# Performance work log

Hardware: AMD Instinct MI355X
Metric: run time of the kernel (lower is better)

## Reference

```python
import jax, jax.numpy as jnp
import numpy as np

DIM = 128
KS = 7
HEADS = 4
HEAD_DIM = DIM // HEADS


def setup_inputs() -> dict:
    key = jax.random.key(0)
    ks = jax.random.split(key, 10)
    B, H, W, C = 4, 64, 64, DIM
    s = 0.02
    return {
        "x": jax.random.normal(ks[0], (B, H, W, C), jnp.float32),
        "qkv_w": jax.random.normal(ks[1], (C, 3 * C), jnp.float32) * s,
        "qkv_b": jnp.zeros((3 * C,), jnp.float32),
        "proj_w": jax.random.normal(ks[2], (C, C), jnp.float32) * s,
        "proj_b": jnp.zeros((C,), jnp.float32),
        "rpb": jax.random.normal(ks[3], (HEADS, 2 * KS - 1, 2 * KS - 1), jnp.float32) * s,
        "g1_w": jax.random.normal(ks[4], (C, C // 2), jnp.float32) * s,
        "g1_b": jnp.zeros((C // 2,), jnp.float32),
        "g2_w": jax.random.normal(ks[5], (C // 2, 1), jnp.float32) * s,
        "g2_b": jnp.zeros((1,), jnp.float32),
    }


def _neighborhood_attention(x, qkv_w, qkv_b, proj_w, proj_b, rpb):
    B, H, W, C = x.shape
    k = KS
    # qkv projection -> [B,H,W,3,heads,head_dim]
    qkv = (x @ qkv_w + qkv_b).reshape(B, H, W, 3, HEADS, HEAD_DIM)
    q = qkv[..., 0, :, :] * (HEAD_DIM ** -0.5)  # [B,H,W,h,d]
    kk = qkv[..., 1, :, :]
    v = qkv[..., 2, :, :]

    # Clamped sliding-window start indices (NATTEN semantics)
    sh = jnp.clip(jnp.arange(H) - k // 2, 0, H - k)  # [H]
    sw = jnp.clip(jnp.arange(W) - k // 2, 0, W - k)  # [W]
    idx_h = sh[:, None] + jnp.arange(k)[None, :]  # [H,k]
    idx_w = sw[:, None] + jnp.arange(k)[None, :]  # [W,k]

    # Gather neighborhood windows: [B,H,W,k,k,h,d]
    kwin = kk[:, idx_h[:, None, :, None], idx_w[None, :, None, :]]
    vwin = v[:, idx_h[:, None, :, None], idx_w[None, :, None, :]]

    # Relative position bias indices: (neighbor - query) + (k-1)
    bih = idx_h - jnp.arange(H)[:, None] + (k - 1)  # [H,k]
    biw = idx_w - jnp.arange(W)[:, None] + (k - 1)  # [W,k]
    # bias: [h,H,W,k,k] -> [H,W,h,k,k]
    bias = rpb[:, bih[:, None, :, None], biw[None, :, None, :]]
    bias = jnp.transpose(bias, (1, 2, 0, 3, 4))

    # scores: [B,H,W,h,k,k]
    scores = jnp.einsum('bxyhd,bxyklhd->bxyhkl', q, kwin) + bias[None]
    attn = jax.nn.softmax(scores.reshape(B, H, W, HEADS, k * k), axis=-1)
    attn = attn.reshape(B, H, W, HEADS, k, k)
    out = jnp.einsum('bxyhkl,bxyklhd->bxyhd', attn, vwin).reshape(B, H, W, C)
    return out @ proj_w + proj_b


def reference(x, qkv_w, qkv_b, proj_w, proj_b, rpb, g1_w, g1_b, g2_w, g2_b):
    attn_out = _neighborhood_attention(x, qkv_w, qkv_b, proj_w, proj_b, rpb)
    gate = jax.nn.sigmoid(jax.nn.relu(x @ g1_w + g1_b) @ g2_w + g2_b)  # [B,H,W,1]
    return attn_out * gate + x
```

## Files before the change

### kernel.cpp

```cpp
#include <hip/hip_runtime.h>
#include <hip/hip_bf16.h>
#include <math.h>

#define PIXELS 16384
#define C      128
#define KS     7
#define HEADS  4
#define HD     32
#define QSCALE 0.17677669529663687f

typedef __bf16 bf16x8 __attribute__((ext_vector_type(8)));
typedef float  f32x4  __attribute__((ext_vector_type(4)));

__device__ inline unsigned short f2bf(float f) {
    unsigned int u = __builtin_bit_cast(unsigned int, f);
    u += 0x7FFFu + ((u >> 16) & 1u);
    return (unsigned short)(u >> 16);
}
__device__ inline float bflo(unsigned int u) {
    return __builtin_bit_cast(float, u << 16);
}
__device__ inline float bfhi(unsigned int u) {
    return __builtin_bit_cast(float, u & 0xFFFF0000u);
}

__global__ __launch_bounds__(256) void prep_kernel(
    const float* __restrict__ x, const float* __restrict__ qkv_w,
    const float* __restrict__ g1_w, const float* __restrict__ qkv_b,
    const float* __restrict__ g1_b, const float* __restrict__ proj_w,
    unsigned short* __restrict__ xb, unsigned short* __restrict__ wT,
    unsigned short* __restrict__ pT, float* __restrict__ bias_ext)
{
    const int blk = blockIdx.x, tid = threadIdx.x;
    if (blk < 2048) {
        int base = blk * 1024 + tid * 4;
        float4 v = *(const float4*)(x + base);
        ushort4 o; o.x = f2bf(v.x); o.y = f2bf(v.y); o.z = f2bf(v.z); o.w = f2bf(v.w);
        *(ushort4*)(xb + base) = o;
    } else if (blk < 2104) {
        int n = (blk - 2048) * 8 + (tid >> 5);
        int kq = tid & 31;
        float f0, f1, f2, f3;
        if (n < 384) {
            f0 = qkv_w[(kq*4+0)*384 + n]; f1 = qkv_w[(kq*4+1)*384 + n];
            f2 = qkv_w[(kq*4+2)*384 + n]; f3 = qkv_w[(kq*4+3)*384 + n];
        } else {
            int nn = n - 384;
            f0 = g1_w[(kq*4+0)*64 + nn]; f1 = g1_w[(kq*4+1)*64 + nn];
            f2 = g1_w[(kq*4+2)*64 + nn]; f3 = g1_w[(kq*4+3)*64 + nn];
        }
        ushort4 o; o.x = f2bf(f0); o.y = f2bf(f1); o.z = f2bf(f2); o.w = f2bf(f3);
        *(ushort4*)(wT + n*128 + kq*4) = o;
    } else if (blk < 2120) {
        int n = (blk - 2104) * 8 + (tid >> 5);
        int kq = tid & 31;
        ushort4 o;
        o.x = f2bf(proj_w[(kq*4+0)*128 + n]);
        o.y = f2bf(proj_w[(kq*4+1)*128 + n]);
        o.z = f2bf(proj_w[(kq*4+2)*128 + n]);
        o.w = f2bf(proj_w[(kq*4+3)*128 + n]);
        *(ushort4*)(pT + n*128 + kq*4) = o;
    } else {
        for (int idx = tid; idx < 448; idx += 256)
            bias_ext[idx] = (idx < 384) ? qkv_b[idx] : g1_b[idx - 384];
    }
}

__global__ __launch_bounds__(256) void gemm_qkvh_fused(
    const unsigned short* __restrict__ xb, const unsigned short* __restrict__ wT,
    const float* __restrict__ bias_ext, const float* __restrict__ g2_w,
    const float* __restrict__ g2_b, unsigned short* __restrict__ qkvb,
    float* __restrict__ gate)
{
    __shared__ __align__(16) unsigned short As[64*128];
    __shared__ __align__(16) unsigned short Bs[64*128];
    const int nt = blockIdx.x;
    const int n0 = nt * 64;
    const int m0 = blockIdx.y * 64;
    const int tid = threadIdx.x;

#pragma unroll
    for (int it = 0; it < 4; it++) {
        int idx = tid + it*256, row = idx >> 4, c = idx & 15;
        uint4 v = *(const uint4*)(xb + (size_t)(m0+row)*128 + c*8);
        *(uint4*)(As + row*128 + ((c ^ (row&7)) << 3)) = v;
    }
#pragma unroll
    for (int it = 0; it < 4; it++) {
        int idx = tid + it*256, row = idx >> 4, c = idx & 15;
        uint4 v = *(const uint4*)(wT + (size_t)(n0+row)*128 + c*8);
        *(uint4*)(Bs + row*128 + ((c ^ (row&7)) << 3)) = v;
    }
    __syncthreads();

    const int wave = tid >> 6, lane = tid & 63;
    const int l15 = lane & 15, quad = lane >> 4;
    const int wm = (wave & 1) * 32, wn = (wave >> 1) * 32;

    f32x4 acc[2][2] = {};
#pragma unroll
    for (int ks = 0; ks < 4; ks++) {
        bf16x8 af[2], bq[2];
#pragma unroll
        for (int mt = 0; mt < 2; mt++) {
            int m = wm + mt*16 + l15;
            af[mt] = *(const bf16x8*)(As + m*128 + (((ks*4+quad) ^ (m&7)) << 3));
        }
#pragma unroll
        for (int ntl = 0; ntl < 2; ntl++) {
            int n = wn + ntl*16 + l15;
            bq[ntl] = *(const bf16x8*)(Bs + n*128 + (((ks*4+quad) ^ (n&7)) << 3));
        }
#pragma unroll
        for (int mt = 0; mt < 2; mt++)
#pragma unroll
            for (int ntl = 0; ntl < 2; ntl++)
                acc[mt][ntl] = __builtin_amdgcn_mfma_f32_16x16x32_bf16(
                    af[mt], bq[ntl], acc[mt][ntl], 0, 0, 0);
    }
    __syncthreads();

    if (nt < 6) {
        unsigned short* Cs = (unsigned short*)As;
#pragma unroll
        for (int ntl = 0; ntl < 2; ntl++) {
            int nl = wn + ntl*16 + l15;
            int ng = n0 + nl;
            float qs = (ng < 128) ? QSCALE : 1.0f;
            float bv = bias_ext[ng];
#pragma unroll
            for (int mt = 0; mt < 2; mt++)
#pragma unroll
                for (int r = 0; r < 4; r++) {
                    int ml = wm + mt*16 + quad*4 + r;
                    Cs[ml*64 + nl] = f2bf((acc[mt][ntl][r] + bv) * qs);
                }
        }
        __syncthreads();
        int row = tid >> 2, part = tid & 3;
        uint4 a = *(const uint4*)(Cs + row*64 + part*16);
        uint4 b = *(const uint4*)(Cs + row*64 + part*16 + 8);
        unsigned short* dst = qkvb + (size_t)(m0+row)*384 + n0 + part*16;
        *(uint4*)dst = a;
        *(uint4*)(dst + 8) = b;
    } else {
        float* gpart = (float*)Bs;
        float rs[2][4];
#pragma unroll
        for (int mt = 0; mt < 2; mt++)
#pragma unroll
            for (int r = 0; r < 4; r++) rs[mt][r] = 0.0f;
#pragma unroll
        for (int ntl = 0; ntl < 2; ntl++) {
            int nl = wn + ntl*16 + l15;
            float bv = bias_ext[384 + nl];
            float gw = g2_w[nl];
#pragma unroll
            for (int mt = 0; mt < 2; mt++)
#pragma unroll
                for (int r = 0; r < 4; r++) {
                    float h = acc[mt][ntl][r] + bv;
                    rs[mt][r] += fmaxf(h, 0.0f) * gw;
                }
        }
#pragma unroll
        for (int off = 1; off <= 8; off <<= 1)
#pragma unroll
            for (int mt = 0; mt < 2; mt++)
#pragma unroll
                for (int r = 0; r < 4; r++)
                    rs[mt][r] += __shfl_xor(rs[mt][r], off);
        if (l15 == 0) {
#pragma unroll
            for (int mt = 0; mt < 2; mt++)
#pragma unroll
                for (int r = 0; r < 4; r++)
                    gpart[(wave >> 1)*64 + wm + mt*16 + quad*4 + r] = rs[mt][r];
        }
        __syncthreads();
        if (tid < 64) {
            float g = gpart[tid] + gpart[64 + tid] + g2_b[0];
            gate[m0 + tid] = 1.0f / (1.0f + __expf(-g));
        }
    }
}

__global__ __launch_bounds__(128) void attn_kernel(
    const unsigned short* __restrict__ qkvb, const float* __restrict__ rpb,
    unsigned short* __restrict__ attnb)
{
    __shared__ __align__(16) unsigned short kvs[196 * 136];
    __shared__ float rpb_lds[2 * 169];

    const int blk = blockIdx.x;
    const int pr = blk & 1;
    const int tile = (blk >> 1) & 63;
    const int b = blk >> 7;
    const int ti0 = (tile >> 3) * 8, tj0 = (tile & 7) * 8;
    int wr0 = ti0 - 3; if (wr0 < 0) wr0 = 0;
    int wc0 = tj0 - 3; if (wc0 < 0) wc0 = 0;

    const int tid = threadIdx.x;

    for (int t = tid; t < 338; t += 128) rpb_lds[t] = rpb[pr * 338 + t];

    for (int idx = tid; idx < 196 * 16; idx += 128) {
        int pos = idx >> 4, t = idx & 15;
        int wr = pos / 14, wc = pos - wr * 14;
        int gr = wr0 + wr; if (gr > 63) gr = 63;
        int gc = wc0 + wc; if (gc > 63) gc = 63;
        size_t gp = (size_t)(((b << 6) + gr) << 6) + gc;
        int src = 128 + ((t >> 3) << 7) + pr * 64 + ((t & 7) << 3);
        uint4 v = *(const uint4*)(qkvb + gp * 384 + src);
        *(uint4*)(kvs + pos * 136 + ((t >> 3) << 6) + ((t & 7) << 3)) = v;
    }
    __syncthreads();

    const int hh = tid >> 6, lane = tid & 63;
    const int h = pr * 2 + hh;
    const int pi = lane >> 3, pj = lane & 7;
    const int i = ti0 + pi, j = tj0 + pj;
    int sh = i - 3; sh = sh < 0 ? 0 : (sh > 57 ? 57 : sh);
    int sw = j - 3; sw = sw < 0 ? 0 : (sw > 57 ? 57 : sw);
    const int dr = sh - wr0, dc = sw - wc0;
    const size_t gp = (size_t)(((b << 6) + i) << 6) + j;

    unsigned int qu[16];
    const unsigned short* qptr = qkvb + gp * 384 + h * 32;
    *(uint4*)(qu + 0)  = *(const uint4*)(qptr + 0);
    *(uint4*)(qu + 4)  = *(const uint4*)(qptr + 8);
    *(uint4*)(qu + 8)  = *(const uint4*)(qptr + 16);
    *(uint4*)(qu + 12) = *(const uint4*)(qptr + 24);
    float qf[32];
#pragma unroll
    for (int p = 0; p < 16; p++) {
        qf[2*p]   = bflo(qu[p]);
        qf[2*p+1] = bfhi(qu[p]);
    }

    float acc[32];
#pragma unroll
    for (int d = 0; d < 32; d++) acc[d] = 0.0f;
    float ssum = 0.0f;

    const float* rl = rpb_lds + hh * 169;
    const int rbase = (sh - i + 6) * 13 + (sw - j + 6);
    const int hwbase = (dr * 14 + dc) * 136 + hh * 32;

    for (int kr = 0; kr < 7; kr++) {
        int hw = hwbase + kr * (14 * 136);
        int ri = rbase + kr * 13;
#pragma unroll
        for (int kc = 0; kc < 7; kc++) {
            const unsigned short* kp = kvs + hw;
            unsigned int ku[16];
            *(uint4*)(ku + 0)  = *(const uint4*)(kp + 0);
            *(uint4*)(ku + 4)  = *(const uint4*)(kp + 8);
            *(uint4*)(ku + 8)  = *(const uint4*)(kp + 16);
            *(uint4*)(ku + 12) = *(const uint4*)(kp + 24);
            float s0 = rl[ri + kc], s1 = 0.0f;
#pragma unroll
            for (int p = 0; p < 8; p++) {
                s0 += qf[2*p]      * bflo(ku[p])     + qf[2*p+1]  * bfhi(ku[p]);
                s1 += qf[2*p+16]   * bflo(ku[p+8])   + qf[2*p+17] * bfhi(ku[p+8]);
            }
            float e = __expf(s0 + s1);
            ssum += e;
            unsigned int vu[16];
            *(uint4*)(vu + 0)  = *(const uint4*)(kp + 64);
            *(uint4*)(vu + 4)  = *(const uint4*)(kp + 72);
            *(uint4*)(vu + 8)  = *(const uint4*)(kp + 80);
            *(uint4*)(vu + 12) = *(const uint4*)(kp + 88);
#pragma unroll
            for (int p = 0; p < 16; p++) {
                acc[2*p]   += e * bflo(vu[p]);
                acc[2*p+1] += e * bfhi(vu[p]);
            }
            hw += 136;
        }
    }

    const float inv = 1.0f / ssum;
    unsigned int o[16];
#pragma unroll
    for (int p = 0; p < 16; p++) {
        unsigned int lo = f2bf(acc[2*p] * inv);
        unsigned int hi = f2bf(acc[2*p+1] * inv);
        o[p] = lo | (hi << 16);
    }
    unsigned short* op = attnb + gp * 128 + h * 32;
    *(uint4*)(op + 0)  = *(const uint4*)(o + 0);
    *(uint4*)(op + 8)  = *(const uint4*)(o + 4);
    *(uint4*)(op + 16) = *(const uint4*)(o + 8);
    *(uint4*)(op + 24) = *(const uint4*)(o + 12);
}

__global__ __launch_bounds__(256) void gemm_proj_mfma(
    const unsigned short* __restrict__ ab, const unsigned short* __restrict__ pT,
    const float* __restrict__ proj_b, const float* __restrict__ gate,
    const float* __restrict__ x, float* __restrict__ out)
{
    __shared__ __align__(16) unsigned short As[64*128];
    __shared__ __align__(16) unsigned short Bs[64*128];
    const int n0 = blockIdx.x * 64;
    const int m0 = blockIdx.y * 64;
    const int tid = threadIdx.x;

#pragma unroll
    for (int it = 0; it < 4; it++) {
        int idx = tid + it*256, row = idx >> 4, c = idx & 15;
        uint4 v = *(const uint4*)(ab + (size_t)(m0+row)*128 + c*8);
        *(uint4*)(As + row*128 + ((c ^ (row&7)) << 3)) = v;
    }
#pragma unroll
    for (int it = 0; it < 4; it++) {
        int idx = tid + it*256, row = idx >> 4, c = idx & 15;
        uint4 v = *(const uint4*)(pT + (size_t)(n0+row)*128 + c*8);
        *(uint4*)(Bs + row*128 + ((c ^ (row&7)) << 3)) = v;
    }
    __syncthreads();

    const int wave = tid >> 6, lane = tid & 63;
    const int l15 = lane & 15, quad = lane >> 4;
    const int wm = (wave & 1) * 32, wn = (wave >> 1) * 32;

    f32x4 acc[2][2] = {};
#pragma unroll
    for (int ks = 0; ks < 4; ks++) {
        bf16x8 af[2], bq[2];
#pragma unroll
        for (int mt = 0; mt < 2; mt++) {
            int m = wm + mt*16 + l15;
            af[mt] = *(const bf16x8*)(As + m*128 + (((ks*4+quad) ^ (m&7)) << 3));
        }
#pragma unroll
        for (int ntl = 0; ntl < 2; ntl++) {
            int n = wn + ntl*16 + l15;
            bq[ntl] = *(const bf16x8*)(Bs + n*128 + (((ks*4+quad) ^ (n&7)) << 3));
        }
#pragma unroll
        for (int mt = 0; mt < 2; mt++)
#pragma unroll
            for (int ntl = 0; ntl < 2; ntl++)
                acc[mt][ntl] = __builtin_amdgcn_mfma_f32_16x16x32_bf16(
                    af[mt], bq[ntl], acc[mt][ntl], 0, 0, 0);
    }
    __syncthreads();

    float* Cs = (float*)As;
#pragma unroll
    for (int ntl = 0; ntl < 2; ntl++) {
        int nl = wn + ntl*16 + l15;
        float bv = proj_b[n0 + nl];
#pragma unroll
        for (int mt = 0; mt < 2; mt++)
#pragma unroll
            for (int r = 0; r < 4; r++) {
                int ml = wm + mt*16 + quad*4 + r;
                Cs[ml*64 + nl] = acc[mt][ntl][r] + bv;
            }
    }
    __syncthreads();
    int row = tid >> 2, part = tid & 3;
    float gv = gate[m0 + row];
    const float* xr = x + (size_t)(m0+row)*128 + n0 + part*16;
    float* orow = out + (size_t)(m0+row)*128 + n0 + part*16;
#pragma unroll
    for (int q = 0; q < 4; q++) {
        float4 cv = *(const float4*)(Cs + row*64 + part*16 + q*4);
        float4 xv = *(const float4*)(xr + q*4);
        float4 o;
        o.x = cv.x * gv + xv.x; o.y = cv.y * gv + xv.y;
        o.z = cv.z * gv + xv.z; o.w = cv.w * gv + xv.w;
        *(float4*)(orow + q*4) = o;
    }
}

extern "C" void kernel_launch(void* const* d_in, const int* in_sizes, int n_in,
                              void* d_out, int out_size, void* d_ws, size_t ws_size,
                              hipStream_t stream)
{
    const float* x      = (const float*)d_in[0];
    const float* qkv_w  = (const float*)d_in[1];
    const float* qkv_b  = (const float*)d_in[2];
    const float* proj_w = (const float*)d_in[3];
    const float* proj_b = (const float*)d_in[4];
    const float* rpb    = (const float*)d_in[5];
    const float* g1_w   = (const float*)d_in[6];
    const float* g1_b   = (const float*)d_in[7];
    const float* g2_w   = (const float*)d_in[8];
    const float* g2_b   = (const float*)d_in[9];
    float* out = (float*)d_out;

    float* ws        = (float*)d_ws;
    float* gate      = ws;
    float* bias_ext  = gate + 16384;
    unsigned short* xb    = (unsigned short*)(bias_ext + 448);
    unsigned short* wT    = xb + 2097152;
    unsigned short* pT    = wT + 57344;
    unsigned short* qkvb  = pT + 16384;
    unsigned short* attnb = qkvb + 6291456;

    (void)in_sizes; (void)n_in; (void)out_size; (void)ws_size;

    prep_kernel<<<2121, 256, 0, stream>>>(x, qkv_w, g1_w, qkv_b, g1_b, proj_w,
                                          xb, wT, pT, bias_ext);
    gemm_qkvh_fused<<<dim3(7, 256), 256, 0, stream>>>(xb, wT, bias_ext,
                                                      g2_w, g2_b, qkvb, gate);
    attn_kernel<<<512, 128, 0, stream>>>(qkvb, rpb, attnb);
    gemm_proj_mfma<<<dim3(2, 256), 256, 0, stream>>>(attnb, pT, proj_b, gate, x, out);
}
```

Measured before the change: 125.1 us.

## Split attention per head per block and divide window rows across two waves

Each attention block now handles a single head instead of a head pair, so twice as many blocks launch and each stages half as much K/V into LDS. The two waves in a block split the seven kernel rows between them, and partial sums are combined through LDS. The QK dot product uses the bf16 fdot2 builtin when it is available. The aim is more parallelism and occupancy plus cheaper score math, at the cost of an extra LDS reduction, a second barrier, and one idle wave during the final write.

```diff
diff --git a/kernel.cpp b/kernel.cpp
--- a/kernel.cpp
+++ b/kernel.cpp
@@ -10,6 +10,7 @@
 #define QSCALE 0.17677669529663687f
 
 typedef __bf16 bf16x8 __attribute__((ext_vector_type(8)));
+typedef __bf16 bf16x2 __attribute__((ext_vector_type(2)));
 typedef float  f32x4  __attribute__((ext_vector_type(4)));
 
 __device__ inline unsigned short f2bf(float f) {
@@ -189,35 +190,34 @@
     const unsigned short* __restrict__ qkvb, const float* __restrict__ rpb,
     unsigned short* __restrict__ attnb)
 {
-    __shared__ __align__(16) unsigned short kvs[196 * 136];
-    __shared__ float rpb_lds[2 * 169];
+    __shared__ __align__(16) unsigned short kvs[196 * 68];
+    __shared__ float rpb_lds[169];
 
     const int blk = blockIdx.x;
-    const int pr = blk & 1;
-    const int tile = (blk >> 1) & 63;
-    const int b = blk >> 7;
-    const int ti0 = (tile >> 3) * 8, tj0 = (tile & 7) * 8;
+    const int h = blk & 3;
+    const int tile = (blk >> 2) & 63;
+    const int b = blk >> 8;
+    const int ti0 = ((tile >> 3) << 3), tj0 = ((tile & 7) << 3);
     int wr0 = ti0 - 3; if (wr0 < 0) wr0 = 0;
     int wc0 = tj0 - 3; if (wc0 < 0) wc0 = 0;
 
     const int tid = threadIdx.x;
 
-    for (int t = tid; t < 338; t += 128) rpb_lds[t] = rpb[pr * 338 + t];
-
-    for (int idx = tid; idx < 196 * 16; idx += 128) {
-        int pos = idx >> 4, t = idx & 15;
+    for (int t = tid; t < 169; t += 128) rpb_lds[t] = rpb[h * 169 + t];
+
+    for (int idx = tid; idx < 196 * 8; idx += 128) {
+        int pos = idx >> 3, t = idx & 7;
         int wr = pos / 14, wc = pos - wr * 14;
         int gr = wr0 + wr; if (gr > 63) gr = 63;
         int gc = wc0 + wc; if (gc > 63) gc = 63;
         size_t gp = (size_t)(((b << 6) + gr) << 6) + gc;
-        int src = 128 + ((t >> 3) << 7) + pr * 64 + ((t & 7) << 3);
+        int src = 128 + ((t >> 2) << 7) + h * 32 + ((t & 3) << 3);
         uint4 v = *(const uint4*)(qkvb + gp * 384 + src);
-        *(uint4*)(kvs + pos * 136 + ((t >> 3) << 6) + ((t & 7) << 3)) = v;
-    }
-    __syncthreads();
-
-    const int hh = tid >> 6, lane = tid & 63;
-    const int h = pr * 2 + hh;
+        *(uint4*)(kvs + pos * 68 + ((t >> 2) << 5) + ((t & 3) << 3)) = v;
+    }
+    __syncthreads();
+
+    const int ww = tid >> 6, lane = tid & 63;
     const int pi = lane >> 3, pj = lane & 7;
     const int i = ti0 + pi, j = tj0 + pj;
     int sh = i - 3; sh = sh < 0 ? 0 : (sh > 57 ? 57 : sh);
@@ -231,68 +231,77 @@
     *(uint4*)(qu + 4)  = *(const uint4*)(qptr + 8);
     *(uint4*)(qu + 8)  = *(const uint4*)(qptr + 16);
     *(uint4*)(qu + 12) = *(const uint4*)(qptr + 24);
-    float qf[32];
-#pragma unroll
-    for (int p = 0; p < 16; p++) {
-        qf[2*p]   = bflo(qu[p]);
-        qf[2*p+1] = bfhi(qu[p]);
-    }
 
     float acc[32];
 #pragma unroll
     for (int d = 0; d < 32; d++) acc[d] = 0.0f;
     float ssum = 0.0f;
 
-    const float* rl = rpb_lds + hh * 169;
     const int rbase = (sh - i + 6) * 13 + (sw - j + 6);
-    const int hwbase = (dr * 14 + dc) * 136 + hh * 32;
-
-    for (int kr = 0; kr < 7; kr++) {
-        int hw = hwbase + kr * (14 * 136);
-        int ri = rbase + kr * 13;
+
+    for (int kr = ww; kr < 7; kr += 2) {
+        const unsigned short* rowp = kvs + ((dr + kr) * 14 + dc) * 68;
+        const float* rl = rpb_lds + rbase + kr * 13;
 #pragma unroll
         for (int kc = 0; kc < 7; kc++) {
-            const unsigned short* kp = kvs + hw;
+            const unsigned short* kp = rowp + kc * 68;
             unsigned int ku[16];
             *(uint4*)(ku + 0)  = *(const uint4*)(kp + 0);
             *(uint4*)(ku + 4)  = *(const uint4*)(kp + 8);
             *(uint4*)(ku + 8)  = *(const uint4*)(kp + 16);
             *(uint4*)(ku + 12) = *(const uint4*)(kp + 24);
-            float s0 = rl[ri + kc], s1 = 0.0f;
-#pragma unroll
-            for (int p = 0; p < 8; p++) {
-                s0 += qf[2*p]      * bflo(ku[p])     + qf[2*p+1]  * bfhi(ku[p]);
-                s1 += qf[2*p+16]   * bflo(ku[p+8])   + qf[2*p+17] * bfhi(ku[p+8]);
-            }
-            float e = __expf(s0 + s1);
+            float s = rl[kc];
+#if __has_builtin(__builtin_amdgcn_fdot2_f32_bf16)
+#pragma unroll
+            for (int p = 0; p < 16; p++)
+                s = __builtin_amdgcn_fdot2_f32_bf16(
+                        __builtin_bit_cast(bf16x2, qu[p]),
+                        __builtin_bit_cast(bf16x2, ku[p]), s, false);
+#else
+#pragma unroll
+            for (int p = 0; p < 16; p++)
+                s += bflo(qu[p]) * bflo(ku[p]) + bfhi(qu[p]) * bfhi(ku[p]);
+#endif
+            float e = __expf(s);
             ssum += e;
             unsigned int vu[16];
-            *(uint4*)(vu + 0)  = *(const uint4*)(kp + 64);
-            *(uint4*)(vu + 4)  = *(const uint4*)(kp + 72);
-            *(uint4*)(vu + 8)  = *(const uint4*)(kp + 80);
-            *(uint4*)(vu + 12) = *(const uint4*)(kp + 88);
+            *(uint4*)(vu + 0)  = *(const uint4*)(kp + 32);
+            *(uint4*)(vu + 4)  = *(const uint4*)(kp + 40);
+            *(uint4*)(vu + 8)  = *(const uint4*)(kp + 48);
+            *(uint4*)(vu + 12) = *(const uint4*)(kp + 56);
 #pragma unroll
             for (int p = 0; p < 16; p++) {
                 acc[2*p]   += e * bflo(vu[p]);
                 acc[2*p+1] += e * bfhi(vu[p]);
             }
-            hw += 136;
-        }
-    }
-
-    const float inv = 1.0f / ssum;
-    unsigned int o[16];
-#pragma unroll
-    for (int p = 0; p < 16; p++) {
-        unsigned int lo = f2bf(acc[2*p] * inv);
-        unsigned int hi = f2bf(acc[2*p+1] * inv);
-        o[p] = lo | (hi << 16);
-    }
-    unsigned short* op = attnb + gp * 128 + h * 32;
-    *(uint4*)(op + 0)  = *(const uint4*)(o + 0);
-    *(uint4*)(op + 8)  = *(const uint4*)(o + 4);
-    *(uint4*)(op + 16) = *(const uint4*)(o + 8);
-    *(uint4*)(op + 24) = *(const uint4*)(o + 12);
+        }
+    }
+
+    float* part = (float*)kvs;
+    __syncthreads();
+    if (ww == 1) {
+#pragma unroll
+        for (int k = 0; k < 8; k++)
+            *(f32x4*)(part + lane*36 + 4*k) = *(const f32x4*)(acc + 4*k);
+        part[lane*36 + 32] = ssum;
+    }
+    __syncthreads();
+    if (ww == 0) {
+        float st = ssum + part[lane*36 + 32];
+        const float inv = 1.0f / st;
+        unsigned int o[16];
+#pragma unroll
+        for (int p = 0; p < 16; p++) {
+            float lo = (acc[2*p]   + part[lane*36 + 2*p])   * inv;
+            float hi = (acc[2*p+1] + part[lane*36 + 2*p+1]) * inv;
+            o[p] = (unsigned int)f2bf(lo) | ((unsigned int)f2bf(hi) << 16);
+        }
+        unsigned short* op = attnb + gp * 128 + h * 32;
+        *(uint4*)(op + 0)  = *(const uint4*)(o + 0);
+        *(uint4*)(op + 8)  = *(const uint4*)(o + 4);
+        *(uint4*)(op + 16) = *(const uint4*)(o + 8);
+        *(uint4*)(op + 24) = *(const uint4*)(o + 12);
+    }
 }
 
 __global__ __launch_bounds__(256) void gemm_proj_mfma(
@@ -407,6 +416,6 @@
                                           xb, wT, pT, bias_ext);
     gemm_qkvh_fused<<<dim3(7, 256), 256, 0, stream>>>(xb, wT, bias_ext,
                                                       g2_w, g2_b, qkvb, gate);
-    attn_kernel<<<512, 128, 0, stream>>>(qkvb, rpb, attnb);
+    attn_kernel<<<1024, 128, 0, stream>>>(qkvb, rpb, attnb);
     gemm_proj_mfma<<<dim3(2, 256), 256, 0, stream>>>(attnb, pT, proj_b, gate, x, out);
 }
```

Result: slower. 154.3 us (+23.4%).
